# Kernel optimization log

Hardware: AMD Instinct MI355X
Metric: run time of the kernel (lower is better)

## Reference

```python
import jax, jax.numpy as jnp
import numpy as np

EPS = 1e-12
SLOPE = 0.2          # LeakyReLU negative slope
N_KNN = (16, 16)     # args.n_knn
TOPK = (2, 2)        # args.topk
MHC = 32             # atten_multi_head_c

def _lin(x, w):
    # VNLinear: contract channel dim (axis 1); x: [B,Cin,3,...] w: [Cout,Cin]
    return jnp.einsum('oc,bc...->bo...', w, x)

def vn_lin_lrelu(x, w, wd):
    # VNLinearAndLeakyReLU: linear + vector-neuron leaky relu with learned direction
    x = _lin(x, w)
    d = _lin(x, wd)
    dot = (x * d).sum(2, keepdims=True)
    dsq = (d * d).sum(2, keepdims=True)
    x_neg = x - (dot / (dsq + EPS)) * d
    return SLOPE * x + (1.0 - SLOPE) * jnp.where(dot >= 0, x, x_neg)

def chnorm(x):
    # channel_equi_vec_normalize: unit 3-vectors scaled by channel-normalized norms
    n = jnp.linalg.norm(x, axis=2, keepdims=True)
    x_dir = x / jnp.maximum(n, EPS)
    cn = jnp.linalg.norm(n, axis=1, keepdims=True)
    return x_dir * (n / jnp.maximum(cn, EPS))

def get_graph_feature(x, k):
    # x: [B,C,3,N] -> [B,2C,3,N,k]; knn on flattened [B,3C,N] coordinates
    B, C, _, N = x.shape
    xf = x.reshape(B, C * 3, N)
    xx = (xf * xf).sum(1)                              # [B,N]
    inner = jnp.einsum('bdn,bdm->bnm', xf, xf)
    neg_dist = 2.0 * inner - xx[:, :, None] - xx[:, None, :]
    _, idx = jax.lax.top_k(neg_dist, k)                # [B,N,k]
    xt = jnp.transpose(x, (0, 3, 1, 2))                # [B,N,C,3]
    nbr = jax.vmap(lambda t, i: t[i])(xt, idx)         # [B,N,k,C,3]
    ctr = jnp.broadcast_to(xt[:, :, None], nbr.shape)
    feat = jnp.concatenate([nbr - ctr, ctr], axis=3)   # [B,N,k,2C,3]
    return jnp.transpose(feat, (0, 3, 4, 1, 2))

def vn_dgcnn(x, w, wd, k):
    # edge conv then mean pool over neighbors
    return vn_lin_lrelu(get_graph_feature(x, k), w, wd).mean(-1)

def cross_context(x, y, qw, qd, kw, kd, vw, vd, knn_k):
    Qx = chnorm(vn_lin_lrelu(x, qw, qd))               # [B,C,3,N]
    yg = get_graph_feature(y, knn_k)                   # [B,2C,3,N,K]
    Ky = chnorm(vn_lin_lrelu(yg, kw, kd))              # [B,C,3,N,K]
    Vy = vn_lin_lrelu(yg, vw, vd)
    qk = jnp.einsum('bcdnk,bcdn->bcnk', Ky, Qx)        # [B,C,N,K]
    B, C, N, K = qk.shape
    nh = C // MHC
    logits = qk.reshape(B, nh, MHC, N, K).sum(2) / jnp.sqrt(jnp.float32(3 * MHC))
    att = jnp.repeat(jax.nn.softmax(logits, axis=-1), MHC, axis=1)  # [B,C,N,K]
    return x + jnp.einsum('bcnk,bcdnk->bcdn', att, Vy)

def _hegn(fx, fy, blocks, h_w, h_d):
    fx = fx[:, None]   # [B,1,3,N]
    fy = fy[:, None]
    fx_blocks, fy_blocks = [], []
    for i, (dg_w, dg_d, qw, qd, kw, kd, vw, vd, gw, gd) in enumerate(blocks):
        fx = vn_dgcnn(fx, dg_w, dg_d, N_KNN[i])
        fy = vn_dgcnn(fy, dg_w, dg_d, N_KNN[i])
        fx = cross_context(fx, fy, qw, qd, kw, kd, vw, vd, N_KNN[i])
        fy = cross_context(fy, fx, qw, qd, kw, kd, vw, vd, N_KNN[i])  # uses updated fx, as in torch
        Fxg = jnp.broadcast_to(fx.mean(-1, keepdims=True), fx.shape)
        Fyg = jnp.broadcast_to(fy.mean(-1, keepdims=True), fy.shape)
        fx = vn_lin_lrelu(jnp.concatenate([fx, Fxg], 1), gw, gd)
        fy = vn_lin_lrelu(jnp.concatenate([fy, Fyg], 1), gw, gd)
        fx_par = fx.mean(1, keepdims=True)             # [B,1,3,N]
        fy_par = fy.mean(1, keepdims=True)
        fx_par = fx_par / jnp.sqrt((fx_par ** 2).sum())  # torch.norm over whole tensor
        fy_par = fy_par / jnp.sqrt((fy_par ** 2).sum())
        phi_x = jnp.einsum('bcdn,bdn->bnc', fx, fx_par[:, 0])
        phi_y = jnp.einsum('bcdn,bdn->bnc', fy, fy_par[:, 0])
        Sc = jax.nn.softmax((phi_x * phi_y).sum(-1), axis=-1)   # [B,N]
        _, idx = jax.lax.top_k(Sc, Sc.shape[1] // TOPK[i])
        fx = jnp.take_along_axis(fx, idx[:, None, None, :], axis=-1)
        fy = jnp.take_along_axis(fy, idx[:, None, None, :], axis=-1)
        fx_blocks.append(fx.mean(-1))
        fy_blocks.append(fy.mean(-1))
    Fx = vn_lin_lrelu(jnp.concatenate(fx_blocks, 1), h_w, h_d)  # [B,32,3]
    Fy = vn_lin_lrelu(jnp.concatenate(fy_blocks, 1), h_w, h_d)
    H = jnp.einsum('bcd,bce->bde', Fx, Fy)                      # [B,3,3]
    u, s, vh = jnp.linalg.svd(H, full_matrices=False)
    R = u @ jnp.swapaxes(vh, -1, -2)   # torch code computes U @ V (v = vh^T)
    S = jnp.linalg.norm(Fy, axis=1) / jnp.linalg.norm(Fx, axis=1)  # [B,3]
    return R, S

def setup_inputs():
    key = jax.random.key(0)
    ks = jax.random.split(key, 26)
    def w(k, o, i):
        return jax.random.normal(k, (o, i), dtype=jnp.float32) / np.float32(np.sqrt(i))
    B, N, C = 2, 2048, 64
    return dict(
        fx=jax.random.normal(ks[0], (B, 3, N), dtype=jnp.float32),
        fy=jax.random.normal(ks[1], (B, 3, N), dtype=jnp.float32),
        dg_w0=w(ks[2], C, 2), dg_d0=w(ks[3], C, C),
        q_w0=w(ks[4], C, C), q_d0=w(ks[5], C, C),
        k_w0=w(ks[6], C, 2 * C), k_d0=w(ks[7], C, C),
        v_w0=w(ks[8], C, 2 * C), v_d0=w(ks[9], C, C),
        g_w0=w(ks[10], C, 2 * C), g_d0=w(ks[11], C, C),
        dg_w1=w(ks[12], C, 2 * C), dg_d1=w(ks[13], C, C),
        q_w1=w(ks[14], C, C), q_d1=w(ks[15], C, C),
        k_w1=w(ks[16], C, 2 * C), k_d1=w(ks[17], C, C),
        v_w1=w(ks[18], C, 2 * C), v_d1=w(ks[19], C, C),
        g_w1=w(ks[20], C, 2 * C), g_d1=w(ks[21], C, C),
        h_w=w(ks[22], 32, 2 * C), h_d=w(ks[23], 32, 32),
    )

def reference(fx, fy, dg_w0, dg_d0, q_w0, q_d0, k_w0, k_d0, v_w0, v_d0, g_w0, g_d0,
              dg_w1, dg_d1, q_w1, q_d1, k_w1, k_d1, v_w1, v_d1, g_w1, g_d1, h_w, h_d):
    blocks = [
        (dg_w0, dg_d0, q_w0, q_d0, k_w0, k_d0, v_w0, v_d0, g_w0, g_d0),
        (dg_w1, dg_d1, q_w1, q_d1, k_w1, k_d1, v_w1, v_d1, g_w1, g_d1),
    ]
    return _hegn(fx, fy, blocks, h_w, h_d)
```

## Files before the change

kernel.cpp:

```cpp
#include <hip/hip_runtime.h>
#include <math.h>

#define SLOPE 0.2f
#define EPSV 1e-12f
#define NEGINF (-3.0e38f)

static __device__ __forceinline__ float lrelu_combine(float xv, float dvv, float dot, float dsq) {
  float xneg = xv - dot / (dsq + EPSV) * dvv;
  float w = (dot >= 0.f) ? xv : xneg;
  return SLOPE * xv + (1.f - SLOPE) * w;
}

__global__ void k_xx2(const float* __restrict__ x0, const float* __restrict__ x1,
                      float* __restrict__ xxA, float* __restrict__ xxB, int D, int N) {
  int side = blockIdx.z;
  const float* x = side ? x1 : x0;
  float* xx = side ? xxB : xxA;
  int b = blockIdx.y;
  int m = blockIdx.x * 256 + threadIdx.x;
  if (m >= N) return;
  const float* xp = x + (size_t)b * D * N + m;
  float s = 0.f;
  for (int d = 0; d < D; ++d) { float v = xp[(size_t)d * N]; s = fmaf(v, v, s); }
  xx[b * N + m] = s;
}

template <int D>
__global__ void __launch_bounds__(256) k_knn2(const float* __restrict__ x0, const float* __restrict__ x1,
                                              const float* __restrict__ xxA, const float* __restrict__ xxB,
                                              int* __restrict__ idx0, int* __restrict__ idx1, int N) {
  int side = blockIdx.z;
  const float* x = side ? x1 : x0;
  const float* xx = side ? xxB : xxA;
  int* idx = side ? idx1 : idx0;
  __shared__ float qt[D * 4];
  __shared__ float dist[4][2048];
  __shared__ float xxq[4];
  int b = blockIdx.y, tid = threadIdx.x;
  int q0 = blockIdx.x * 4;
  const float* xb = x + (size_t)b * D * N;
  for (int i = tid; i < D * 4; i += 256) qt[i] = xb[(size_t)(i >> 2) * N + q0 + (i & 3)];
  if (tid < 4) xxq[tid] = xx[b * N + q0 + tid];
  __syncthreads();
  int kouter = N >> 10;
  for (int k = 0; k < kouter; ++k) {
    int m0 = tid + (k << 10);
    float4 a0 = {0, 0, 0, 0}, a1 = {0, 0, 0, 0}, a2 = {0, 0, 0, 0}, a3 = {0, 0, 0, 0};
#pragma unroll
    for (int d = 0; d < D; ++d) {
      const float4 q4 = *(const float4*)&qt[d * 4];
      const float* xr = xb + (size_t)d * N + m0;
      float v0 = xr[0], v1 = xr[256], v2 = xr[512], v3 = xr[768];
      a0.x = fmaf(q4.x, v0, a0.x); a0.y = fmaf(q4.y, v0, a0.y);
      a0.z = fmaf(q4.z, v0, a0.z); a0.w = fmaf(q4.w, v0, a0.w);
      a1.x = fmaf(q4.x, v1, a1.x); a1.y = fmaf(q4.y, v1, a1.y);
      a1.z = fmaf(q4.z, v1, a1.z); a1.w = fmaf(q4.w, v1, a1.w);
      a2.x = fmaf(q4.x, v2, a2.x); a2.y = fmaf(q4.y, v2, a2.y);
      a2.z = fmaf(q4.z, v2, a2.z); a2.w = fmaf(q4.w, v2, a2.w);
      a3.x = fmaf(q4.x, v3, a3.x); a3.y = fmaf(q4.y, v3, a3.y);
      a3.z = fmaf(q4.z, v3, a3.z); a3.w = fmaf(q4.w, v3, a3.w);
    }
    const float* xxb2 = xx + b * N + m0;
    float x0v = xxb2[0], x1v = xxb2[256], x2v = xxb2[512], x3v = xxb2[768];
    dist[0][m0]       = 2.f * a0.x - xxq[0] - x0v;
    dist[1][m0]       = 2.f * a0.y - xxq[1] - x0v;
    dist[2][m0]       = 2.f * a0.z - xxq[2] - x0v;
    dist[3][m0]       = 2.f * a0.w - xxq[3] - x0v;
    dist[0][m0 + 256] = 2.f * a1.x - xxq[0] - x1v;
    dist[1][m0 + 256] = 2.f * a1.y - xxq[1] - x1v;
    dist[2][m0 + 256] = 2.f * a1.z - xxq[2] - x1v;
    dist[3][m0 + 256] = 2.f * a1.w - xxq[3] - x1v;
    dist[0][m0 + 512] = 2.f * a2.x - xxq[0] - x2v;
    dist[1][m0 + 512] = 2.f * a2.y - xxq[1] - x2v;
    dist[2][m0 + 512] = 2.f * a2.z - xxq[2] - x2v;
    dist[3][m0 + 512] = 2.f * a2.w - xxq[3] - x2v;
    dist[0][m0 + 768] = 2.f * a3.x - xxq[0] - x3v;
    dist[1][m0 + 768] = 2.f * a3.y - xxq[1] - x3v;
    dist[2][m0 + 768] = 2.f * a3.z - xxq[2] - x3v;
    dist[3][m0 + 768] = 2.f * a3.w - xxq[3] - x3v;
  }
  __syncthreads();
  int g = tid >> 6, lane = tid & 63;
  float* dr = dist[g];
  int n = q0 + g;
  int imax = N >> 8;
  int* op = idx + ((size_t)b * N + n) * 16;
  for (int r = 0; r < 16; ++r) {
    float bv = NEGINF;
    int bi = N;
    for (int i = 0; i < imax; ++i) {
      int mb = i * 256 + lane * 4;
      float4 v = *(const float4*)&dr[mb];
      if (v.x > bv) { bv = v.x; bi = mb; }
      if (v.y > bv) { bv = v.y; bi = mb + 1; }
      if (v.z > bv) { bv = v.z; bi = mb + 2; }
      if (v.w > bv) { bv = v.w; bi = mb + 3; }
    }
#pragma unroll
    for (int s = 1; s < 64; s <<= 1) {
      float ov = __shfl_xor(bv, s, 64);
      int oi = __shfl_xor(bi, s, 64);
      if (ov > bv || (ov == bv && oi < bi)) { bv = ov; bi = oi; }
    }
    if (lane == 0) { op[r] = bi; dr[bi] = NEGINF; }
  }
}

template <int D>
__global__ void __launch_bounds__(256) k_gram(const float* __restrict__ x0, const float* __restrict__ x1,
                                              const float* __restrict__ xxA, const float* __restrict__ xxB,
                                              float* __restrict__ dist, int N) {
  int side = blockIdx.z;
  const float* x = side ? x1 : x0;
  const float* xx = side ? xxB : xxA;
  __shared__ float sq[16][64];
  __shared__ float sm[16][64];
  int qtiles = N >> 6;
  int b = blockIdx.y / qtiles;
  int qt = blockIdx.y - b * qtiles;
  int m0 = blockIdx.x << 6;
  int q0 = qt << 6;
  int tid = threadIdx.x;
  int tmg = tid & 15, tqg = tid >> 4;
  const float* xb = x + (size_t)b * D * N;
  float acc[16];
#pragma unroll
  for (int i = 0; i < 16; ++i) acc[i] = 0.f;
  for (int dc = 0; dc < D; dc += 16) {
    for (int i = tid; i < 1024; i += 256) {
      int dd = i >> 6, c = i & 63;
      sq[dd][c] = xb[(size_t)(dc + dd) * N + q0 + c];
      sm[dd][c] = xb[(size_t)(dc + dd) * N + m0 + c];
    }
    __syncthreads();
#pragma unroll
    for (int dd = 0; dd < 16; ++dd) {
      float4 qv = *(const float4*)&sq[dd][tqg * 4];
      float4 mv = *(const float4*)&sm[dd][tmg * 4];
      acc[0]  = fmaf(qv.x, mv.x, acc[0]);
      acc[1]  = fmaf(qv.x, mv.y, acc[1]);
      acc[2]  = fmaf(qv.x, mv.z, acc[2]);
      acc[3]  = fmaf(qv.x, mv.w, acc[3]);
      acc[4]  = fmaf(qv.y, mv.x, acc[4]);
      acc[5]  = fmaf(qv.y, mv.y, acc[5]);
      acc[6]  = fmaf(qv.y, mv.z, acc[6]);
      acc[7]  = fmaf(qv.y, mv.w, acc[7]);
      acc[8]  = fmaf(qv.z, mv.x, acc[8]);
      acc[9]  = fmaf(qv.z, mv.y, acc[9]);
      acc[10] = fmaf(qv.z, mv.z, acc[10]);
      acc[11] = fmaf(qv.z, mv.w, acc[11]);
      acc[12] = fmaf(qv.w, mv.x, acc[12]);
      acc[13] = fmaf(qv.w, mv.y, acc[13]);
      acc[14] = fmaf(qv.w, mv.z, acc[14]);
      acc[15] = fmaf(qv.w, mv.w, acc[15]);
    }
    __syncthreads();
  }
  float4 xxm = *(const float4*)&xx[b * N + m0 + tmg * 4];
#pragma unroll
  for (int qi = 0; qi < 4; ++qi) {
    int q = q0 + tqg * 4 + qi;
    float xq = xx[b * N + q];
    float4 o;
    o.x = 2.f * acc[qi * 4 + 0] - xq - xxm.x;
    o.y = 2.f * acc[qi * 4 + 1] - xq - xxm.y;
    o.z = 2.f * acc[qi * 4 + 2] - xq - xxm.z;
    o.w = 2.f * acc[qi * 4 + 3] - xq - xxm.w;
    *(float4*)&dist[((size_t)((side * 2 + b) * N + q)) * N + m0 + tmg * 4] = o;
  }
}

__global__ void __launch_bounds__(256) k_sel(const float* __restrict__ dist,
                                             int* __restrict__ idx0, int* __restrict__ idx1, int N) {
  int side = blockIdx.z;
  int* idx = side ? idx1 : idx0;
  __shared__ float dr4[4][2048];
  int b = blockIdx.y, tid = threadIdx.x;
  int q0 = blockIdx.x * 4;
  for (int g2 = 0; g2 < 4; ++g2) {
    const float* row = dist + ((size_t)((side * 2 + b) * N + q0 + g2)) * N;
    for (int m = tid; m < N; m += 256) dr4[g2][m] = row[m];
  }
  __syncthreads();
  int g = tid >> 6, lane = tid & 63;
  float* dr = dr4[g];
  int n = q0 + g;
  int imax = N >> 8;
  int* op = idx + ((size_t)b * N + n) * 16;
  for (int r = 0; r < 16; ++r) {
    float bv = NEGINF;
    int bi = N;
    for (int i = 0; i < imax; ++i) {
      int mb = i * 256 + lane * 4;
      float4 v = *(const float4*)&dr[mb];
      if (v.x > bv) { bv = v.x; bi = mb; }
      if (v.y > bv) { bv = v.y; bi = mb + 1; }
      if (v.z > bv) { bv = v.z; bi = mb + 2; }
      if (v.w > bv) { bv = v.w; bi = mb + 3; }
    }
#pragma unroll
    for (int s = 1; s < 64; s <<= 1) {
      float ov = __shfl_xor(bv, s, 64);
      int oi = __shfl_xor(bi, s, 64);
      if (ov > bv || (ov == bv && oi < bi)) { bv = ov; bi = oi; }
    }
    if (lane == 0) { op[r] = bi; dr[bi] = NEGINF; }
  }
}

struct LinSlots {
  const float* W[5]; const float* X[5]; const float* bias[5];
  float* cm[5]; float* pm[5];
  int ws[5]; int woff[5]; int sub[5];
};

template <int KT>
__global__ void __launch_bounds__(256) k_linm(LinSlots S, int N) {
  __shared__ float wl[64 * ((KT + 3) & ~3)];
  const int KP = (KT + 3) & ~3;
  int slot = blockIdx.z >> 2;
  int oc = (blockIdx.z & 3) * 16;
  const float* W = S.W[slot];
  int ws = S.ws[slot], woff = S.woff[slot], sub = S.sub[slot];
  int tid = threadIdx.x;
  for (int i = tid; i < 64 * KT; i += 256) {
    int o = i / KT, k = i - o * KT;
    float v = W[o * ws + woff + k];
    if (sub) v -= W[o * ws + k];
    wl[o * KP + k] = v;
  }
  __syncthreads();
  int b = blockIdx.y;
  int j = blockIdx.x * 256 + tid;
  int M3 = 3 * N;
  if (j >= M3) return;
  const float* Xb = S.X[slot] + (size_t)b * KT * M3;
  float xv[KT];
#pragma unroll
  for (int k = 0; k < KT; ++k) xv[k] = Xb[(size_t)k * M3 + j];
  int d = j / N;
  const float* bias = S.bias[slot];
  float acc[16];
  if (bias) {
#pragma unroll
    for (int oo = 0; oo < 16; ++oo) acc[oo] = bias[b * 192 + (oc + oo) * 3 + d];
  } else {
#pragma unroll
    for (int oo = 0; oo < 16; ++oo) acc[oo] = 0.f;
  }
#pragma unroll
  for (int oo = 0; oo < 16; ++oo) {
    const float* wr = &wl[(oc + oo) * KP];
    float s = acc[oo];
#pragma unroll
    for (int k = 0; k < KT; ++k) s = fmaf(wr[k], xv[k], s);
    acc[oo] = s;
  }
  if (S.cm[slot]) {
    float* ob = S.cm[slot] + (size_t)b * 64 * M3;
#pragma unroll
    for (int oo = 0; oo < 16; ++oo) ob[(size_t)(oc + oo) * M3 + j] = acc[oo];
  }
  if (S.pm[slot]) {
    int n = j - d * N;
    float4* pp = (float4*)(S.pm[slot] + ((size_t)((b * N + n) * 3 + d)) * 64 + oc);
    pp[0] = make_float4(acc[0], acc[1], acc[2], acc[3]);
    pp[1] = make_float4(acc[4], acc[5], acc[6], acc[7]);
    pp[2] = make_float4(acc[8], acc[9], acc[10], acc[11]);
    pp[3] = make_float4(acc[12], acc[13], acc[14], acc[15]);
  }
}

__global__ void __launch_bounds__(256) k_edge2(const float* __restrict__ P1a, const float* __restrict__ P2a,
                                               const float* __restrict__ D1a, const float* __restrict__ D2a,
                                               const float* __restrict__ P1b, const float* __restrict__ P2b,
                                               const float* __restrict__ D1b, const float* __restrict__ D2b,
                                               const int* __restrict__ idxA, const int* __restrict__ idxB,
                                               float* __restrict__ outA, float* __restrict__ outB, int N) {
  int side = blockIdx.y;
  const float* P1 = side ? P1b : P1a;
  const float* P2 = side ? P2b : P2a;
  const float* D1 = side ? D1b : D1a;
  const float* D2 = side ? D2b : D2a;
  const int* idx = side ? idxB : idxA;
  float* out = side ? outB : outA;
  int tid = threadIdx.x;
  int p = blockIdx.x * 4 + (tid >> 6);
  int c = tid & 63;
  int b = p / N, n = p - b * N;
  size_t bn = ((size_t)(b * N + n) * 3) * 64 + c;
  float p2[3], d2[3];
#pragma unroll
  for (int d = 0; d < 3; ++d) { p2[d] = P2[bn + d * 64]; d2[d] = D2[bn + d * 64]; }
  const int* ip = idx + ((size_t)b * N + n) * 16;
  float acc0 = 0.f, acc1 = 0.f, acc2 = 0.f;
  for (int j = 0; j < 16; ++j) {
    int m = ip[j];
    size_t bm = ((size_t)(b * N + m) * 3) * 64 + c;
    float xl[3], dv[3];
#pragma unroll
    for (int d = 0; d < 3; ++d) {
      xl[d] = P1[bm + d * 64] + p2[d];
      dv[d] = D1[bm + d * 64] + d2[d];
    }
    float dot = xl[0] * dv[0] + xl[1] * dv[1] + xl[2] * dv[2];
    float dsq = dv[0] * dv[0] + dv[1] * dv[1] + dv[2] * dv[2];
    acc0 += lrelu_combine(xl[0], dv[0], dot, dsq);
    acc1 += lrelu_combine(xl[1], dv[1], dot, dsq);
    acc2 += lrelu_combine(xl[2], dv[2], dot, dsq);
  }
  size_t r0 = (size_t)((b * 64 + c) * 3) * N;
  out[r0 + n] = acc0 * (1.f / 16.f);
  out[r0 + N + n] = acc1 * (1.f / 16.f);
  out[r0 + 2 * (size_t)N + n] = acc2 * (1.f / 16.f);
}

__global__ void __launch_bounds__(256) k_qfin(const float* __restrict__ XL, const float* __restrict__ DV,
                                              float* __restrict__ outpm, int N) {
  int tid = threadIdx.x;
  int p = blockIdx.x * 4 + (tid >> 6);
  int c = tid & 63;
  int b = p / N, n = p - b * N;
  size_t bn = ((size_t)(b * N + n) * 3) * 64 + c;
  float xl[3], dv[3];
#pragma unroll
  for (int d = 0; d < 3; ++d) { xl[d] = XL[bn + d * 64]; dv[d] = DV[bn + d * 64]; }
  float dot = xl[0] * dv[0] + xl[1] * dv[1] + xl[2] * dv[2];
  float dsq = dv[0] * dv[0] + dv[1] * dv[1] + dv[2] * dv[2];
  float z[3];
#pragma unroll
  for (int d = 0; d < 3; ++d) z[d] = lrelu_combine(xl[d], dv[d], dot, dsq);
  float n2 = z[0] * z[0] + z[1] * z[1] + z[2] * z[2];
  float cn2 = n2;
#pragma unroll
  for (int s = 1; s < 64; s <<= 1) cn2 += __shfl_xor(cn2, s, 64);
  float n_o = sqrtf(n2), cn = sqrtf(cn2);
  float scl = (n_o / fmaxf(cn, EPSV)) / fmaxf(n_o, EPSV);
#pragma unroll
  for (int d = 0; d < 3; ++d) outpm[bn + d * 64] = z[d] * scl;
}

__global__ void __launch_bounds__(256) k_att(const float* __restrict__ xres,
                                             const float* __restrict__ qxpm,
                                             const float* __restrict__ KP1, const float* __restrict__ KP2,
                                             const float* __restrict__ KD1, const float* __restrict__ KD2,
                                             const float* __restrict__ VP1, const float* __restrict__ VP2,
                                             const float* __restrict__ VD1, const float* __restrict__ VD2,
                                             const int* __restrict__ idx,
                                             float* __restrict__ out, int N) {
  int tid = threadIdx.x;
  int p = blockIdx.x * 4 + (tid >> 6);
  int c = tid & 63;
  int b = p / N, n = p - b * N;
  size_t bn = ((size_t)(b * N + n) * 3) * 64 + c;
  float qv[3], kp2[3], kd2[3], vp2[3], vd2[3];
#pragma unroll
  for (int d = 0; d < 3; ++d) {
    qv[d] = qxpm[bn + d * 64];
    kp2[d] = KP2[bn + d * 64];
    kd2[d] = KD2[bn + d * 64];
    vp2[d] = VP2[bn + d * 64];
    vd2[d] = VD2[bn + d * 64];
  }
  const int* ip = idx + ((size_t)b * N + n) * 16;
  float l[16];
#pragma unroll
  for (int j = 0; j < 16; ++j) {
    int m = ip[j];
    size_t bm = ((size_t)(b * N + m) * 3) * 64 + c;
    float xl[3], dv[3];
#pragma unroll
    for (int d = 0; d < 3; ++d) {
      xl[d] = KP1[bm + d * 64] + kp2[d];
      dv[d] = KD1[bm + d * 64] + kd2[d];
    }
    float dot = xl[0] * dv[0] + xl[1] * dv[1] + xl[2] * dv[2];
    float dsq = dv[0] * dv[0] + dv[1] * dv[1] + dv[2] * dv[2];
    float z[3];
#pragma unroll
    for (int d = 0; d < 3; ++d) z[d] = lrelu_combine(xl[d], dv[d], dot, dsq);
    float n2 = z[0] * z[0] + z[1] * z[1] + z[2] * z[2];
    float cn2 = n2;
#pragma unroll
    for (int s = 1; s < 64; s <<= 1) cn2 += __shfl_xor(cn2, s, 64);
    float n_o = sqrtf(n2), cn = sqrtf(cn2);
    float scl = (n_o / fmaxf(cn, EPSV)) / fmaxf(n_o, EPSV);
    float part = (z[0] * qv[0] + z[1] * qv[1] + z[2] * qv[2]) * scl;
#pragma unroll
    for (int s = 1; s < 32; s <<= 1) part += __shfl_xor(part, s, 32);
    part = __shfl(part, 0, 32);
    l[j] = part * 0.102062072615966f;
  }
  float mx = l[0];
#pragma unroll
  for (int j = 1; j < 16; ++j) mx = fmaxf(mx, l[j]);
  float sum = 0.f;
#pragma unroll
  for (int j = 0; j < 16; ++j) { l[j] = expf(l[j] - mx); sum += l[j]; }
  float inv = 1.f / sum;
#pragma unroll
  for (int j = 0; j < 16; ++j) l[j] *= inv;
  float acc0 = 0.f, acc1 = 0.f, acc2 = 0.f;
#pragma unroll
  for (int j = 0; j < 16; ++j) {
    int m = ip[j];
    float av = l[j];
    size_t bm = ((size_t)(b * N + m) * 3) * 64 + c;
    float xl[3], dv[3];
#pragma unroll
    for (int d = 0; d < 3; ++d) {
      xl[d] = VP1[bm + d * 64] + vp2[d];
      dv[d] = VD1[bm + d * 64] + vd2[d];
    }
    float dot = xl[0] * dv[0] + xl[1] * dv[1] + xl[2] * dv[2];
    float dsq = dv[0] * dv[0] + dv[1] * dv[1] + dv[2] * dv[2];
    acc0 = fmaf(av, lrelu_combine(xl[0], dv[0], dot, dsq), acc0);
    acc1 = fmaf(av, lrelu_combine(xl[1], dv[1], dot, dsq), acc1);
    acc2 = fmaf(av, lrelu_combine(xl[2], dv[2], dot, dsq), acc2);
  }
  size_t r0 = (size_t)((b * 64 + c) * 3) * N;
  out[r0 + n] = xres[r0 + n] + acc0;
  out[r0 + N + n] = xres[r0 + N + n] + acc1;
  out[r0 + 2 * (size_t)N + n] = xres[r0 + 2 * (size_t)N + n] + acc2;
}

__global__ void __launch_bounds__(256) k_gfin(const float* __restrict__ XLa, const float* __restrict__ DVa,
                                              const float* __restrict__ XLb, const float* __restrict__ DVb,
                                              float* __restrict__ outa, float* __restrict__ outpa,
                                              float* __restrict__ outb, float* __restrict__ outpb, int N) {
  int side = blockIdx.y;
  const float* XL = side ? XLb : XLa;
  const float* DV = side ? DVb : DVa;
  float* out = side ? outb : outa;
  float* outpm = side ? outpb : outpa;
  int tid = threadIdx.x;
  int p = blockIdx.x * 4 + (tid >> 6);
  int c = tid & 63;
  int b = p / N, n = p - b * N;
  size_t bn = ((size_t)(b * N + n) * 3) * 64 + c;
  float xl[3], dv[3];
#pragma unroll
  for (int d = 0; d < 3; ++d) { xl[d] = XL[bn + d * 64]; dv[d] = DV[bn + d * 64]; }
  float dot = xl[0] * dv[0] + xl[1] * dv[1] + xl[2] * dv[2];
  float dsq = dv[0] * dv[0] + dv[1] * dv[1] + dv[2] * dv[2];
  size_t r0 = (size_t)((b * 64 + c) * 3) * N;
#pragma unroll
  for (int d = 0; d < 3; ++d) {
    float z = lrelu_combine(xl[d], dv[d], dot, dsq);
    out[r0 + (size_t)d * N + n] = z;
    outpm[bn + d * 64] = z;
  }
}

__global__ void k_gbias2(const float* __restrict__ gw, const float* __restrict__ meanX,
                         const float* __restrict__ meanY,
                         float* __restrict__ cbX, float* __restrict__ cbY) {
  int b = blockIdx.x, which = blockIdx.y, tid = threadIdx.x;
  int o = tid / 3, d = tid - o * 3;
  const float* mb = (which ? meanY : meanX) + b * 192;
  float* cb = (which ? cbY : cbX);
  float s = 0.f;
  for (int c = 0; c < 64; ++c) s = fmaf(gw[o * 128 + 64 + c], mb[c * 3 + d], s);
  cb[b * 192 + tid] = s;
}

__global__ void k_cmean2(const float* __restrict__ x1, const float* __restrict__ x2,
                         float* __restrict__ o1, float* __restrict__ o2,
                         int N, int ostride, int obase, float inv) {
  __shared__ float red[256];
  int b = blockIdx.y, cd = blockIdx.x, which = blockIdx.z, tid = threadIdx.x;
  const float* x = which ? x2 : x1;
  float* out = which ? o2 : o1;
  const float* p = x + ((size_t)b * 192 + cd) * N;
  float s = 0.f;
  for (int i = tid; i < N; i += 256) s += p[i];
  red[tid] = s;
  __syncthreads();
  for (int st = 128; st > 0; st >>= 1) {
    if (tid < st) red[tid] += red[tid + st];
    __syncthreads();
  }
  if (tid == 0) out[(size_t)b * ostride + obase + cd] = red[0] * inv;
}

__global__ void k_parmean(const float* __restrict__ fx, const float* __restrict__ fy,
                          float* __restrict__ px, float* __restrict__ py, int N, int B) {
  int gi = blockIdx.x * 256 + threadIdx.x;
  int total = B * 3 * N;
  if (gi >= total) return;
  int b = gi / (3 * N);
  int r = gi - b * 3 * N;
  const float* fxb = fx + (size_t)b * 192 * N + r;
  const float* fyb = fy + (size_t)b * 192 * N + r;
  float sx = 0.f, sy = 0.f;
  for (int c = 0; c < 64; ++c) { sx += fxb[(size_t)c * 3 * N]; sy += fyb[(size_t)c * 3 * N]; }
  px[gi] = sx * (1.f / 64.f);
  py[gi] = sy * (1.f / 64.f);
}

__global__ void k_dotphi(const float* __restrict__ fx, const float* __restrict__ fy,
                         const float* __restrict__ px, const float* __restrict__ py,
                         float* __restrict__ dps, int N, int B) {
  int gi = blockIdx.x * 256 + threadIdx.x;
  if (gi >= B * N) return;
  int b = gi / N, n = gi - b * N;
  const float* fxb = fx + (size_t)b * 192 * N + n;
  const float* fyb = fy + (size_t)b * 192 * N + n;
  const float* pxb = px + (size_t)b * 3 * N + n;
  const float* pyb = py + (size_t)b * 3 * N + n;
// ... 273 lines not shown
      if (idir == 1) {
        double cs = 1.0, oldcs = 1.0, sn = 0.0, oldsn = 0.0, r;
        for (int i = ll; i <= m - 1; ++i) {
          dlartg_(d[i - 1] * cs, e[i - 1], &cs, &sn, &r);
          if (i > ll) e[i - 2] = oldsn * r;
          dlartg_(oldcs * r, d[i] * sn, &oldcs, &oldsn, &d[i - 1]);
          csv[cnt] = cs; snv[cnt] = sn; ocsv[cnt] = oldcs; osnv[cnt] = oldsn; cnt++;
        }
        double hh = d[m - 1] * cs;
        d[m - 1] = hh * oldcs;
        e[m - 2] = hh * oldsn;
        for (int k = 0; k < cnt; ++k) {
          int r0 = ll - 1 + k, r1 = r0 + 1;
          for (int j = 0; j < 3; ++j) {
            double t1 = VT[r0][j], t2 = VT[r1][j];
            VT[r0][j] = snv[k] * t2 + csv[k] * t1;
            VT[r1][j] = csv[k] * t2 - snv[k] * t1;
          }
        }
        for (int k = 0; k < cnt; ++k) {
          int c0 = ll - 1 + k, c1 = c0 + 1;
          for (int i2 = 0; i2 < 3; ++i2) {
            double t1 = U[i2][c0], t2 = U[i2][c1];
            U[i2][c0] = osnv[k] * t2 + ocsv[k] * t1;
            U[i2][c1] = ocsv[k] * t2 - osnv[k] * t1;
          }
        }
        if (fabs(e[m - 2]) <= thresh) e[m - 2] = 0.0;
      } else {
        double cs = 1.0, oldcs = 1.0, sn = 0.0, oldsn = 0.0, r;
        for (int i = m; i >= ll + 1; --i) {
          dlartg_(d[i - 1] * cs, e[i - 2], &cs, &sn, &r);
          if (i < m) e[i - 1] = oldsn * r;
          dlartg_(oldcs * r, d[i - 2] * sn, &oldcs, &oldsn, &d[i - 1]);
          int k = i - ll - 1;
          csv[k] = cs; snv[k] = -sn; ocsv[k] = oldcs; osnv[k] = -oldsn; cnt++;
        }
        double hh = d[ll - 1] * cs;
        d[ll - 1] = hh * oldcs;
        e[ll - 1] = hh * oldsn;
        for (int k = cnt - 1; k >= 0; --k) {
          int r0 = ll - 1 + k, r1 = r0 + 1;
          for (int j = 0; j < 3; ++j) {
            double t1 = VT[r0][j], t2 = VT[r1][j];
            VT[r0][j] = osnv[k] * t2 + ocsv[k] * t1;
            VT[r1][j] = ocsv[k] * t2 - osnv[k] * t1;
          }
        }
        for (int k = cnt - 1; k >= 0; --k) {
          int c0 = ll - 1 + k, c1 = c0 + 1;
          for (int i2 = 0; i2 < 3; ++i2) {
            double t1 = U[i2][c0], t2 = U[i2][c1];
            U[i2][c0] = snv[k] * t2 + csv[k] * t1;
            U[i2][c1] = csv[k] * t2 - snv[k] * t1;
          }
        }
        if (fabs(e[ll - 1]) <= thresh) e[ll - 1] = 0.0;
      }
    } else {
      if (idir == 1) {
        double f = (fabs(d[ll - 1]) - shift) * (copysign(1.0, d[ll - 1]) + shift / d[ll - 1]);
        double g = e[ll - 1];
        double cosr, sinr, cosl2, sinl2, r;
        for (int i = ll; i <= m - 1; ++i) {
          dlartg_(f, g, &cosr, &sinr, &r);
          if (i > ll) e[i - 2] = r;
          f = cosr * d[i - 1] + sinr * e[i - 1];
          e[i - 1] = cosr * e[i - 1] - sinr * d[i - 1];
          g = sinr * d[i];
          d[i] = cosr * d[i];
          dlartg_(f, g, &cosl2, &sinl2, &r);
          d[i - 1] = r;
          f = cosl2 * e[i - 1] + sinl2 * d[i];
          d[i] = cosl2 * d[i] - sinl2 * e[i - 1];
          if (i < m - 1) {
            g = sinl2 * e[i];
            e[i] = cosl2 * e[i];
          }
          csv[cnt] = cosr; snv[cnt] = sinr; ocsv[cnt] = cosl2; osnv[cnt] = sinl2; cnt++;
        }
        e[m - 2] = f;
        for (int k = 0; k < cnt; ++k) {
          int r0 = ll - 1 + k, r1 = r0 + 1;
          for (int j = 0; j < 3; ++j) {
            double t1 = VT[r0][j], t2 = VT[r1][j];
            VT[r0][j] = snv[k] * t2 + csv[k] * t1;
            VT[r1][j] = csv[k] * t2 - snv[k] * t1;
          }
        }
        for (int k = 0; k < cnt; ++k) {
          int c0 = ll - 1 + k, c1 = c0 + 1;
          for (int i2 = 0; i2 < 3; ++i2) {
            double t1 = U[i2][c0], t2 = U[i2][c1];
            U[i2][c0] = osnv[k] * t2 + ocsv[k] * t1;
            U[i2][c1] = ocsv[k] * t2 - osnv[k] * t1;
          }
        }
        if (fabs(e[m - 2]) <= thresh) e[m - 2] = 0.0;
      } else {
        double f = (fabs(d[m - 1]) - shift) * (copysign(1.0, d[m - 1]) + shift / d[m - 1]);
        double g = e[m - 2];
        for (int i = m; i >= ll + 1; --i) {
          double cosr, sinr, cosl2, sinl2, r;
          dlartg_(f, g, &cosr, &sinr, &r);
          if (i < m) e[i - 1] = r;
          f = cosr * d[i - 1] + sinr * e[i - 2];
          e[i - 2] = cosr * e[i - 2] - sinr * d[i - 1];
          g = sinr * d[i - 2];
          d[i - 2] = cosr * d[i - 2];
          dlartg_(f, g, &cosl2, &sinl2, &r);
          d[i - 1] = r;
          f = cosl2 * e[i - 2] + sinl2 * d[i - 2];
          d[i - 2] = cosl2 * d[i - 2] - sinl2 * e[i - 2];
          if (i > ll + 1) {
            g = sinl2 * e[i - 3];
            e[i - 3] = cosl2 * e[i - 3];
          }
          int k = i - ll - 1;
          ocsv[k] = cosl2; osnv[k] = -sinl2; csv[k] = cosr; snv[k] = -sinr; cnt++;
        }
        e[ll - 1] = f;
        for (int k = cnt - 1; k >= 0; --k) {
          int r0 = ll - 1 + k, r1 = r0 + 1;
          for (int j = 0; j < 3; ++j) {
            double t1 = VT[r0][j], t2 = VT[r1][j];
            VT[r0][j] = snv[k] * t2 + csv[k] * t1;
            VT[r1][j] = csv[k] * t2 - snv[k] * t1;
          }
        }
        for (int k = cnt - 1; k >= 0; --k) {
          int c0 = ll - 1 + k, c1 = c0 + 1;
          for (int i2 = 0; i2 < 3; ++i2) {
            double t1 = U[i2][c0], t2 = U[i2][c1];
            U[i2][c0] = osnv[k] * t2 + ocsv[k] * t1;
            U[i2][c1] = ocsv[k] * t2 - osnv[k] * t1;
          }
        }
        if (fabs(e[ll - 1]) <= thresh) e[ll - 1] = 0.0;
      }
    }
  }
  for (int i = 0; i < n; ++i)
    if (d[i] < 0.0) { d[i] = -d[i]; for (int j = 0; j < 3; ++j) VT[i][j] = -VT[i][j]; }
  for (int i = 1; i <= n - 1; ++i) {
    int isub = 1; double smn = d[0];
    for (int j = 2; j <= n + 1 - i; ++j)
      if (d[j - 1] <= smn) { isub = j; smn = d[j - 1]; }
    if (isub != n + 1 - i) {
      int a = isub - 1, b2 = n - i;
      double t = d[a]; d[a] = d[b2]; d[b2] = t;
      for (int j = 0; j < 3; ++j) { t = VT[a][j]; VT[a][j] = VT[b2][j]; VT[b2][j] = t; }
      for (int j = 0; j < 3; ++j) { t = U[j][a]; U[j][a] = U[j][b2]; U[j][b2] = t; }
    }
  }
}

__global__ void k_svd(const float* __restrict__ Fx, const float* __restrict__ Fy,
                      float* __restrict__ out, int B) {
  int b = blockIdx.x;
  if (threadIdx.x != 0) return;
  double A[3][3];
  for (int d = 0; d < 3; ++d)
    for (int e = 0; e < 3; ++e) {
      double s = 0.0;
      for (int c = 0; c < 32; ++c)
        s += (double)Fx[((size_t)b * 32 + c) * 3 + d] * (double)Fy[((size_t)b * 32 + c) * 3 + e];
      A[d][e] = s;
    }
  double dg[3], eg[2], tauq0, tauq1, taup0;
  double v1_1 = 0, v1_2 = 0, v2_1 = 0, w1 = 0;
  {
    double alpha = A[0][0];
    double xn = sqrt(A[1][0] * A[1][0] + A[2][0] * A[2][0]);
    if (xn == 0.0) { tauq0 = 0.0; dg[0] = alpha; }
    else {
      double beta = -copysign(sqrt(alpha * alpha + xn * xn), alpha);
      tauq0 = (beta - alpha) / beta;
      double scal = 1.0 / (alpha - beta);
      v1_1 = A[1][0] * scal; v1_2 = A[2][0] * scal;
      dg[0] = beta;
    }
    for (int j = 1; j < 3; ++j) {
      double w = A[0][j] + v1_1 * A[1][j] + v1_2 * A[2][j];
      w *= tauq0;
      A[0][j] -= w; A[1][j] -= w * v1_1; A[2][j] -= w * v1_2;
    }
  }
  {
    double alpha = A[0][1];
    double xn = fabs(A[0][2]);
    if (xn == 0.0) { taup0 = 0.0; eg[0] = alpha; }
    else {
      double beta = -copysign(sqrt(alpha * alpha + xn * xn), alpha);
      taup0 = (beta - alpha) / beta;
      w1 = A[0][2] / (alpha - beta);
      eg[0] = beta;
    }
    for (int i = 1; i < 3; ++i) {
      double t = A[i][1] + w1 * A[i][2];
      t *= taup0;
      A[i][1] -= t; A[i][2] -= t * w1;
    }
  }
  {
    double alpha = A[1][1];
    double xn = fabs(A[2][1]);
    if (xn == 0.0) { tauq1 = 0.0; dg[1] = alpha; }
    else {
      double beta = -copysign(sqrt(alpha * alpha + xn * xn), alpha);
      tauq1 = (beta - alpha) / beta;
      v2_1 = A[2][1] / (alpha - beta);
      dg[1] = beta;
    }
    double w = A[1][2] + v2_1 * A[2][2];
    w *= tauq1;
    A[1][2] -= w; A[2][2] -= w * v2_1;
  }
  eg[1] = A[1][2];
  dg[2] = A[2][2];
  double U[3][3] = {{1, 0, 0}, {0, 1, 0}, {0, 0, 1}};
  double VT[3][3] = {{1, 0, 0}, {0, 1, 0}, {0, 0, 1}};
  dbdsqr3(dg, eg, VT, U);
  for (int j = 0; j < 3; ++j) {
    double w = U[1][j] + v2_1 * U[2][j];
    w *= tauq1;
    U[1][j] -= w; U[2][j] -= w * v2_1;
  }
  for (int j = 0; j < 3; ++j) {
    double w = U[0][j] + v1_1 * U[1][j] + v1_2 * U[2][j];
    w *= tauq0;
    U[0][j] -= w; U[1][j] -= w * v1_1; U[2][j] -= w * v1_2;
  }
  for (int r = 0; r < 3; ++r) {
    double t = VT[r][1] + w1 * VT[r][2];
    t *= taup0;
    VT[r][1] -= t; VT[r][2] -= t * w1;
  }
  for (int i = 0; i < 3; ++i)
    for (int j = 0; j < 3; ++j) {
      double r = 0;
      for (int k = 0; k < 3; ++k) r += U[i][k] * VT[j][k];
      out[b * 9 + i * 3 + j] = (float)r;
    }
  for (int dd = 0; dd < 3; ++dd) {
    float sx = 0.f, sy = 0.f;
    for (int c = 0; c < 32; ++c) {
      float vx = Fx[((size_t)b * 32 + c) * 3 + dd];
      float vy = Fy[((size_t)b * 32 + c) * 3 + dd];
      sx = fmaf(vx, vx, sx);
      sy = fmaf(vy, vy, sy);
    }
    out[B * 9 + b * 3 + dd] = sqrtf(sy) / sqrtf(sx);
  }
}

extern "C" void kernel_launch(void* const* d_in, const int* in_sizes, int n_in,
                              void* d_out, int out_size, void* d_ws, size_t ws_size,
                              hipStream_t stream) {
  (void)in_sizes; (void)n_in; (void)out_size; (void)ws_size;
  const int B = 2, N0 = 2048;
  const float* W[24];
  for (int i = 0; i < 24; ++i) W[i] = (const float*)d_in[i];

  float* ws = (float*)d_ws;
  const size_t P = (size_t)B * 64 * 3 * 2048;
  float* bufA = ws;
  float* bufB = bufA + P;
  float* bufC = bufB + P;
  float* bufD = bufC + P;
  float* bufApm = bufD + P;
  float* bufBpm = bufApm + P;
  float* qxpm = bufBpm + P;
  float* C1 = qxpm + P;
  float* C2 = C1 + P;
  float* C3 = C2 + P;
  float* C4 = C3 + P;
  float* C5 = C4 + P;
  float* M1 = C5 + P;
  float* M2 = M1 + P;
  float* M3 = M2 + P;
  float* M4 = M3 + P;
  float* M5 = M4 + P;
  float* M6 = M5 + P;
  float* M7 = M6 + P;
  float* M8 = M7 + P;
  float* M9 = M8 + P;
  float* M10 = M9 + P;
  float* px = M10 + P;
  float* py = px + 12288;
  float* dps = py + 12288;
  float* xx0 = dps + 4096;
  float* xx1 = xx0 + 4096;
  float* meanX = xx1 + 4096;
  float* meanY = meanX + 384;
  float* cbX = meanY + 384;
  float* cbY = cbX + 384;
  float* blkX = cbY + 384;
  float* blkY = blkX + 768;
  float* Fxb = blkY + 768;
  float* Fyb = Fxb + 192;
  int* idxA = (int*)(Fyb + 192);
  int* idxB = idxA + 65536;
  int* sel = idxB + 65536;
  float* distb = C1;

  auto knn3 = [&](const float* xa, const float* xb2, int N, int* ia, int* ib, int ns) {
    k_xx2<<<dim3((N + 255) / 256, B, ns), 256, 0, stream>>>(xa, xb2, xx0, xx1, 3, N);
    dim3 g2(N / 4, B, ns);
    k_knn2<3><<<g2, 256, 0, stream>>>(xa, xb2, xx0, xx1, ia, ib, N);
  };
  auto knn192 = [&](const float* xa, const float* xb2, int N, int* ia, int* ib, int ns) {
    k_xx2<<<dim3((N + 255) / 256, B, ns), 256, 0, stream>>>(xa, xb2, xx0, xx1, 192, N);
    int qtiles = N >> 6;
    k_gram<192><<<dim3(qtiles, B * qtiles, ns), 256, 0, stream>>>(xa, xb2, xx0, xx1, distb, N);
    k_sel<<<dim3(N / 4, B, ns), 256, 0, stream>>>(distb, ia, ib, N);
  };

  const float* fx = W[0];
  const float* fy = W[1];
  int N = N0;
  for (int blk = 0; blk < 2; ++blk) {
    const float* dgw = W[blk ? 12 : 2]; const float* dgd = W[blk ? 13 : 3];
    const float* qw  = W[blk ? 14 : 4]; const float* qd  = W[blk ? 15 : 5];
    const float* kw  = W[blk ? 16 : 6]; const float* kd  = W[blk ? 17 : 7];
    const float* vw  = W[blk ? 18 : 8]; const float* vd  = W[blk ? 19 : 9];
    const float* gw  = W[blk ? 20 : 10]; const float* gd = W[blk ? 21 : 11];
    dim3 gP(B * N / 4);
    dim3 gL((3 * N + 255) / 256, B, 1);

    if (blk == 0) knn3(fx, fy, N, idxA, idxB, 2);
    else          knn192(fx, fy, N, idxA, idxB, 2);
    {
      LinSlots s{};
      int wsd = (blk == 0) ? 2 : 128;
      int off2 = (blk == 0) ? 1 : 64;
      const float* Xs[4] = {fx, fx, fy, fy};
      float* cms[4] = {C1, C2, C3, C4};
      float* pms[4] = {M1, M2, M3, M4};
      for (int i = 0; i < 4; ++i) {
        s.W[i] = dgw; s.X[i] = Xs[i]; s.bias[i] = nullptr;
        s.cm[i] = cms[i]; s.pm[i] = pms[i];
        s.ws[i] = wsd; s.woff[i] = (i & 1) ? off2 : 0; s.sub[i] = (i & 1);
      }
      gL.z = 16;
      if (blk == 0) k_linm<1><<<gL, 256, 0, stream>>>(s, N);
      else          k_linm<64><<<gL, 256, 0, stream>>>(s, N);
    }
    {
      LinSlots s{};
      const float* Xs[4] = {C1, C2, C3, C4};
      float* pms[4] = {M5, M6, M7, M8};
      for (int i = 0; i < 4; ++i) {
        s.W[i] = dgd; s.X[i] = Xs[i]; s.bias[i] = nullptr;
        s.cm[i] = nullptr; s.pm[i] = pms[i];
        s.ws[i] = 64; s.woff[i] = 0; s.sub[i] = 0;
      }
      gL.z = 16;
      k_linm<64><<<gL, 256, 0, stream>>>(s, N);
    }
    k_edge2<<<dim3(B * N / 4, 2), 256, 0, stream>>>(M1, M2, M5, M6, M3, M4, M7, M8,
                                                    idxA, idxB, bufA, bufB, N);

    knn192(bufB, bufB, N, idxB, idxB, 1);
    {
      LinSlots s{};
      const float* Wm[5] = {qw, kw, kw, vw, vw};
      const float* Xs[5] = {bufA, bufB, bufB, bufB, bufB};
      float* cms[5] = {C1, C2, C3, C4, C5};
      float* pms[5] = {M1, M3, M4, M5, M6};
      int wss[5] = {64, 128, 128, 128, 128};
      int offs[5] = {0, 0, 64, 0, 64};
      int subs[5] = {0, 0, 1, 0, 1};
      for (int i = 0; i < 5; ++i) {
        s.W[i] = Wm[i]; s.X[i] = Xs[i]; s.bias[i] = nullptr;
        s.cm[i] = cms[i]; s.pm[i] = pms[i];
        s.ws[i] = wss[i]; s.woff[i] = offs[i]; s.sub[i] = subs[i];
      }
      gL.z = 20;
      k_linm<64><<<gL, 256, 0, stream>>>(s, N);
    }
    {
      LinSlots s{};
      const float* Wm[5] = {qd, kd, kd, vd, vd};
      const float* Xs[5] = {C1, C2, C3, C4, C5};
      float* pms[5] = {M2, M7, M8, M9, M10};
      for (int i = 0; i < 5; ++i) {
        s.W[i] = Wm[i]; s.X[i] = Xs[i]; s.bias[i] = nullptr;
        s.cm[i] = nullptr; s.pm[i] = pms[i];
        s.ws[i] = 64; s.woff[i] = 0; s.sub[i] = 0;
      }
      gL.z = 20;
      k_linm<64><<<gL, 256, 0, stream>>>(s, N);
    }
    k_qfin<<<gP, 256, 0, stream>>>(M1, M2, qxpm, N);
    k_att<<<gP, 256, 0, stream>>>(bufA, qxpm, M3, M4, M7, M8, M5, M6, M9, M10, idxB, bufC, N);

    knn192(bufC, bufC, N, idxA, idxA, 1);
    {
      LinSlots s{};
      const float* Wm[5] = {qw, kw, kw, vw, vw};
      const float* Xs[5] = {bufB, bufC, bufC, bufC, bufC};
      float* cms[5] = {C1, C2, C3, C4, C5};
      float* pms[5] = {M1, M3, M4, M5, M6};
      int wss[5] = {64, 128, 128, 128, 128};
      int offs[5] = {0, 0, 64, 0, 64};
      int subs[5] = {0, 0, 1, 0, 1};
      for (int i = 0; i < 5; ++i) {
        s.W[i] = Wm[i]; s.X[i] = Xs[i]; s.bias[i] = nullptr;
        s.cm[i] = cms[i]; s.pm[i] = pms[i];
        s.ws[i] = wss[i]; s.woff[i] = offs[i]; s.sub[i] = subs[i];
      }
      gL.z = 20;
      k_linm<64><<<gL, 256, 0, stream>>>(s, N);
    }
    {
      LinSlots s{};
      const float* Wm[5] = {qd, kd, kd, vd, vd};
      const float* Xs[5] = {C1, C2, C3, C4, C5};
      float* pms[5] = {M2, M7, M8, M9, M10};
      for (int i = 0; i < 5; ++i) {
        s.W[i] = Wm[i]; s.X[i] = Xs[i]; s.bias[i] = nullptr;
        s.cm[i] = nullptr; s.pm[i] = pms[i];
        s.ws[i] = 64; s.woff[i] = 0; s.sub[i] = 0;
      }
      gL.z = 20;
      k_linm<64><<<gL, 256, 0, stream>>>(s, N);
    }
    k_qfin<<<gP, 256, 0, stream>>>(M1, M2, qxpm, N);
    k_att<<<gP, 256, 0, stream>>>(bufB, qxpm, M3, M4, M7, M8, M5, M6, M9, M10, idxA, bufD, N);

    k_cmean2<<<dim3(192, B, 2), 256, 0, stream>>>(bufC, bufD, meanX, meanY, N, 192, 0, 1.f / (float)N);
    k_gbias2<<<dim3(B, 2), 192, 0, stream>>>(gw, meanX, meanY, cbX, cbY);
    {
      LinSlots s{};
      const float* Xs[2] = {bufC, bufD};
      const float* bs[2] = {cbX, cbY};
      float* cms[2] = {C1, C2};
      float* pms[2] = {M1, M2};
      for (int i = 0; i < 2; ++i) {
        s.W[i] = gw; s.X[i] = Xs[i]; s.bias[i] = bs[i];
        s.cm[i] = cms[i]; s.pm[i] = pms[i];
        s.ws[i] = 128; s.woff[i] = 0; s.sub[i] = 0;
      }
      gL.z = 8;
      k_linm<64><<<gL, 256, 0, stream>>>(s, N);
    }
    {
      LinSlots s{};
      const float* Xs[2] = {C1, C2};
      float* pms[2] = {M3, M4};
      for (int i = 0; i < 2; ++i) {
        s.W[i] = gd; s.X[i] = Xs[i]; s.bias[i] = nullptr;
        s.cm[i] = nullptr; s.pm[i] = pms[i];
        s.ws[i] = 64; s.woff[i] = 0; s.sub[i] = 0;
      }
      gL.z = 8;
      k_linm<64><<<gL, 256, 0, stream>>>(s, N);
    }
    k_gfin<<<dim3(B * N / 4, 2), 256, 0, stream>>>(M1, M3, M2, M4, bufA, bufApm, bufB, bufBpm, N);

    int Nh = N / 2;
    k_parmean<<<dim3((B * 3 * N + 255) / 256), 256, 0, stream>>>(bufA, bufB, px, py, N, B);
    k_dotphi<<<dim3((B * N + 255) / 256), 256, 0, stream>>>(bufA, bufB, px, py, dps, N, B);
    k_topsel<<<dim3(B), 1024, 0, stream>>>(dps, sel, N, Nh);
    k_gather<<<dim3(B * Nh / 4), 256, 0, stream>>>(bufApm, bufBpm, sel, bufC, bufD, N, Nh);
    k_cmean2<<<dim3(192, B, 2), 256, 0, stream>>>(bufC, bufD, blkX, blkY, Nh, 384, blk * 192, 1.f / (float)Nh);
    fx = bufC; fy = bufD;
    N = Nh;
  }
  k_head<<<dim3(2, B), 96, 0, stream>>>(blkX, blkY, W[22], W[23], Fxb, Fyb);
  k_svd<<<dim3(B), 64, 0, stream>>>(Fxb, Fyb, (float*)d_out, B);
}
```

Before: 1.419 ms.

## Fuse kNN gram tiles with streaming per-segment top-16 and add merge kernel

Replaces the full gram distance matrix write plus separate selection kernel with a kernel that computes 64x64 distance tiles in shared memory and maintains a running sorted top-16 per query over one quarter of the candidates. A small merge kernel then picks the final 16 from the four partial lists. This removes the large global distance buffer round trip and the repeated 16-pass argmax scans, at the cost of fewer blocks (N/64 x B*4) and serialized ballot-driven insertion work that may be slow early on, when many candidates qualify.

```diff
diff --git a/kernel.cpp b/kernel.cpp
--- a/kernel.cpp
+++ b/kernel.cpp
@@ -106,105 +106,139 @@
   }
 }
 
-template <int D>
-__global__ void __launch_bounds__(256) k_gram(const float* __restrict__ x0, const float* __restrict__ x1,
+__global__ void __launch_bounds__(256) k_knnb(const float* __restrict__ x0, const float* __restrict__ x1,
                                               const float* __restrict__ xxA, const float* __restrict__ xxB,
-                                              float* __restrict__ dist, int N) {
+                                              float* __restrict__ pv, int* __restrict__ pi, int N) {
   int side = blockIdx.z;
   const float* x = side ? x1 : x0;
   const float* xx = side ? xxB : xxA;
   __shared__ float sq[16][64];
   __shared__ float sm[16][64];
-  int qtiles = N >> 6;
-  int b = blockIdx.y / qtiles;
-  int qt = blockIdx.y - b * qtiles;
-  int m0 = blockIdx.x << 6;
-  int q0 = qt << 6;
+  __shared__ float dist[64][64];
+  __shared__ float tv[64][16];
+  __shared__ int   ti[64][16];
+  int b = blockIdx.y >> 2;
+  int seg = blockIdx.y & 3;
+  int q0 = blockIdx.x << 6;
   int tid = threadIdx.x;
+  for (int i = tid; i < 64 * 16; i += 256) { tv[i >> 4][i & 15] = NEGINF; ti[i >> 4][i & 15] = 0x7fffffff; }
+  __syncthreads();
+  const float* xb = x + (size_t)b * 192 * N;
   int tmg = tid & 15, tqg = tid >> 4;
-  const float* xb = x + (size_t)b * D * N;
-  float acc[16];
-#pragma unroll
-  for (int i = 0; i < 16; ++i) acc[i] = 0.f;
-  for (int dc = 0; dc < D; dc += 16) {
-    for (int i = tid; i < 1024; i += 256) {
-      int dd = i >> 6, c = i & 63;
-      sq[dd][c] = xb[(size_t)(dc + dd) * N + q0 + c];
-      sm[dd][c] = xb[(size_t)(dc + dd) * N + m0 + c];
+  int wave = tid >> 6, lane = tid & 63;
+  int segN = N >> 2;
+  int NT = segN >> 6;
+  for (int t = 0; t < NT; ++t) {
+    int m0 = seg * segN + (t << 6);
+    float acc[16];
+#pragma unroll
+    for (int i = 0; i < 16; ++i) acc[i] = 0.f;
+    for (int dc = 0; dc < 192; dc += 16) {
+      for (int i = tid; i < 1024; i += 256) {
+        int dd = i >> 6, c = i & 63;
+        sq[dd][c] = xb[(size_t)(dc + dd) * N + q0 + c];
+        sm[dd][c] = xb[(size_t)(dc + dd) * N + m0 + c];
+      }
+      __syncthreads();
+#pragma unroll
+      for (int dd = 0; dd < 16; ++dd) {
+        float4 qv = *(const float4*)&sq[dd][tqg * 4];
+        float4 mv = *(const float4*)&sm[dd][tmg * 4];
+        acc[0]  = fmaf(qv.x, mv.x, acc[0]);
+        acc[1]  = fmaf(qv.x, mv.y, acc[1]);
+        acc[2]  = fmaf(qv.x, mv.z, acc[2]);
+        acc[3]  = fmaf(qv.x, mv.w, acc[3]);
+        acc[4]  = fmaf(qv.y, mv.x, acc[4]);
+        acc[5]  = fmaf(qv.y, mv.y, acc[5]);
+        acc[6]  = fmaf(qv.y, mv.z, acc[6]);
+        acc[7]  = fmaf(qv.y, mv.w, acc[7]);
+        acc[8]  = fmaf(qv.z, mv.x, acc[8]);
+        acc[9]  = fmaf(qv.z, mv.y, acc[9]);
+        acc[10] = fmaf(qv.z, mv.z, acc[10]);
+        acc[11] = fmaf(qv.z, mv.w, acc[11]);
+        acc[12] = fmaf(qv.w, mv.x, acc[12]);
+        acc[13] = fmaf(qv.w, mv.y, acc[13]);
+        acc[14] = fmaf(qv.w, mv.z, acc[14]);
+        acc[15] = fmaf(qv.w, mv.w, acc[15]);
+      }
+      __syncthreads();
+    }
+    float4 xxm = *(const float4*)&xx[b * N + m0 + tmg * 4];
+#pragma unroll
+    for (int qi = 0; qi < 4; ++qi) {
+      int ql = tqg * 4 + qi;
+      float xq = xx[b * N + q0 + ql];
+      float4 o;
+      o.x = 2.f * acc[qi * 4 + 0] - xq - xxm.x;
+      o.y = 2.f * acc[qi * 4 + 1] - xq - xxm.y;
+      o.z = 2.f * acc[qi * 4 + 2] - xq - xxm.z;
+      o.w = 2.f * acc[qi * 4 + 3] - xq - xxm.w;
+      *(float4*)&dist[ql][tmg * 4] = o;
     }
     __syncthreads();
-#pragma unroll
-    for (int dd = 0; dd < 16; ++dd) {
-      float4 qv = *(const float4*)&sq[dd][tqg * 4];
-      float4 mv = *(const float4*)&sm[dd][tmg * 4];
-      acc[0]  = fmaf(qv.x, mv.x, acc[0]);
-      acc[1]  = fmaf(qv.x, mv.y, acc[1]);
-      acc[2]  = fmaf(qv.x, mv.z, acc[2]);
-      acc[3]  = fmaf(qv.x, mv.w, acc[3]);
-      acc[4]  = fmaf(qv.y, mv.x, acc[4]);
-      acc[5]  = fmaf(qv.y, mv.y, acc[5]);
-      acc[6]  = fmaf(qv.y, mv.z, acc[6]);
-      acc[7]  = fmaf(qv.y, mv.w, acc[7]);
-      acc[8]  = fmaf(qv.z, mv.x, acc[8]);
-      acc[9]  = fmaf(qv.z, mv.y, acc[9]);
-      acc[10] = fmaf(qv.z, mv.z, acc[10]);
-      acc[11] = fmaf(qv.z, mv.w, acc[11]);
-      acc[12] = fmaf(qv.w, mv.x, acc[12]);
-      acc[13] = fmaf(qv.w, mv.y, acc[13]);
-      acc[14] = fmaf(qv.w, mv.z, acc[14]);
-      acc[15] = fmaf(qv.w, mv.w, acc[15]);
+    for (int qq = 0; qq < 16; ++qq) {
+      int ql = wave * 16 + qq;
+      float dv = dist[ql][lane];
+      int mg = m0 + lane;
+      float thv = tv[ql][15];
+      int thi = ti[ql][15];
+      bool qual = (dv > thv) || (dv == thv && mg < thi);
+      unsigned long long mask = __ballot(qual);
+      while (mask) {
+        int src = __ffsll((unsigned long long)mask) - 1;
+        mask &= mask - 1;
+        float cv = __shfl(dv, src, 64);
+        int cm = m0 + src;
+        bool prec = false;
+        if (lane < 16) {
+          float ev = tv[ql][lane];
+          int ei = ti[ql][lane];
+          prec = (ev > cv) || (ev == cv && ei < cm);
+        }
+        unsigned long long pmask = __ballot(prec);
+        int p = __popcll(pmask & 0xFFFFull);
+        if (p < 16) {
+          float upv = 0.f; int upi = 0;
+          if (lane < 16 && lane > p) { upv = tv[ql][lane - 1]; upi = ti[ql][lane - 1]; }
+          if (lane < 16) {
+            if (lane == p) { tv[ql][lane] = cv; ti[ql][lane] = cm; }
+            else if (lane > p) { tv[ql][lane] = upv; ti[ql][lane] = upi; }
+          }
+        }
+      }
     }
     __syncthreads();
   }
-  float4 xxm = *(const float4*)&xx[b * N + m0 + tmg * 4];
-#pragma unroll
-  for (int qi = 0; qi < 4; ++qi) {
-    int q = q0 + tqg * 4 + qi;
-    float xq = xx[b * N + q];
-    float4 o;
-    o.x = 2.f * acc[qi * 4 + 0] - xq - xxm.x;
-    o.y = 2.f * acc[qi * 4 + 1] - xq - xxm.y;
-    o.z = 2.f * acc[qi * 4 + 2] - xq - xxm.z;
-    o.w = 2.f * acc[qi * 4 + 3] - xq - xxm.w;
-    *(float4*)&dist[((size_t)((side * 2 + b) * N + q)) * N + m0 + tmg * 4] = o;
-  }
-}
-
-__global__ void __launch_bounds__(256) k_sel(const float* __restrict__ dist,
-                                             int* __restrict__ idx0, int* __restrict__ idx1, int N) {
+  for (int i = tid; i < 64 * 16; i += 256) {
+    int ql = i >> 4, slot = i & 15;
+    size_t base = ((size_t)((side * 2 + b) * N + q0 + ql)) * 64 + seg * 16;
+    pv[base + slot] = tv[ql][slot];
+    pi[base + slot] = ti[ql][slot];
+  }
+}
+
+__global__ void __launch_bounds__(256) k_kmerge(const float* __restrict__ pv, const int* __restrict__ pi,
+                                                int* __restrict__ idx0, int* __restrict__ idx1, int N) {
   int side = blockIdx.z;
   int* idx = side ? idx1 : idx0;
-  __shared__ float dr4[4][2048];
-  int b = blockIdx.y, tid = threadIdx.x;
-  int q0 = blockIdx.x * 4;
-  for (int g2 = 0; g2 < 4; ++g2) {
-    const float* row = dist + ((size_t)((side * 2 + b) * N + q0 + g2)) * N;
-    for (int m = tid; m < N; m += 256) dr4[g2][m] = row[m];
-  }
-  __syncthreads();
-  int g = tid >> 6, lane = tid & 63;
-  float* dr = dr4[g];
-  int n = q0 + g;
-  int imax = N >> 8;
-  int* op = idx + ((size_t)b * N + n) * 16;
+  int b = blockIdx.y;
+  int tid = threadIdx.x;
+  int q = blockIdx.x * 4 + (tid >> 6);
+  int lane = tid & 63;
+  size_t base = ((size_t)((side * 2 + b) * N + q)) * 64;
+  float v = pv[base + lane];
+  int i = pi[base + lane];
+  int* op = idx + ((size_t)b * N + q) * 16;
   for (int r = 0; r < 16; ++r) {
-    float bv = NEGINF;
-    int bi = N;
-    for (int i = 0; i < imax; ++i) {
-      int mb = i * 256 + lane * 4;
-      float4 v = *(const float4*)&dr[mb];
-      if (v.x > bv) { bv = v.x; bi = mb; }
-      if (v.y > bv) { bv = v.y; bi = mb + 1; }
-      if (v.z > bv) { bv = v.z; bi = mb + 2; }
-      if (v.w > bv) { bv = v.w; bi = mb + 3; }
-    }
+    float bv = v; int bi = i;
 #pragma unroll
     for (int s = 1; s < 64; s <<= 1) {
       float ov = __shfl_xor(bv, s, 64);
       int oi = __shfl_xor(bi, s, 64);
       if (ov > bv || (ov == bv && oi < bi)) { bv = ov; bi = oi; }
     }
-    if (lane == 0) { op[r] = bi; dr[bi] = NEGINF; }
+    if (lane == 0) op[r] = bi;
+    if (v == bv && i == bi) { v = NEGINF; i = 0x7fffffff; }
   }
 }
 
@@ -1084,7 +1118,8 @@
   int* idxA = (int*)(Fyb + 192);
   int* idxB = idxA + 65536;
   int* sel = idxB + 65536;
-  float* distb = C1;
+  float* pvb = C1;
+  int* pib = (int*)C2;
 
   auto knn3 = [&](const float* xa, const float* xb2, int N, int* ia, int* ib, int ns) {
     k_xx2<<<dim3((N + 255) / 256, B, ns), 256, 0, stream>>>(xa, xb2, xx0, xx1, 3, N);
@@ -1093,9 +1128,8 @@
   };
   auto knn192 = [&](const float* xa, const float* xb2, int N, int* ia, int* ib, int ns) {
     k_xx2<<<dim3((N + 255) / 256, B, ns), 256, 0, stream>>>(xa, xb2, xx0, xx1, 192, N);
-    int qtiles = N >> 6;
-    k_gram<192><<<dim3(qtiles, B * qtiles, ns), 256, 0, stream>>>(xa, xb2, xx0, xx1, distb, N);
-    k_sel<<<dim3(N / 4, B, ns), 256, 0, stream>>>(distb, ia, ib, N);
+    k_knnb<<<dim3(N >> 6, B * 4, ns), 256, 0, stream>>>(xa, xb2, xx0, xx1, pvb, pib, N);
+    k_kmerge<<<dim3(N / 4, B, ns), 256, 0, stream>>>(pvb, pib, ia, ib, N);
   };
 
   const float* fx = W[0];
```

After: 3.502 ms. 147% more time.
